# Kernel tuning notes

Hardware: AMD Instinct MI355X
Metric: run time of the kernel (lower is better)

## Reference

```python
import jax, jax.numpy as jnp
import numpy as np

BATCH = 1_000_000
D = 20

def setup_inputs() -> dict:
    key = jax.random.key(0)
    kX, kW, kb, kR = jax.random.split(key, 4)
    X = jax.random.normal(kX, (BATCH, D), dtype=jnp.float32)
    W = jax.random.normal(kW, (D, D), dtype=jnp.float32)
    b = jax.random.normal(kb, (D,), dtype=jnp.float32)
    rand_weight = jax.random.uniform(kR, (D, D), dtype=jnp.float32)  # torch.rand, requires_grad=False
    return {"X": X, "W": W, "b": b, "rand_weight": rand_weight}

def reference(X, W, b, rand_weight):
    # X = self.linear(X)
    X1 = X @ W.T + b
    # X = relu(X @ rand_weight + 1)
    X2 = jax.nn.relu(X1 @ rand_weight + 1.0)
    # X = self.linear(X)  (shared weights)
    X3 = X2 @ W.T + b
    # while X.abs().sum() > 1: X = X / 2  -- data-dependent loop, kept on-device
    def cond(Xc):
        return jnp.sum(jnp.abs(Xc)) > 1.0
    def body(Xc):
        return Xc * 0.5
    Xf = jax.lax.while_loop(cond, body, X3)
    return jnp.sum(Xf)
```

## Files before the change

kernel.cpp:

```cpp
#include <hip/hip_runtime.h>
#include <math.h>

#define D 20
#define NROWS 1000000
#define NTILES (NROWS / 16)
#define TPB 256
#define TILES_PER_BLK 16
#define NSB ((NTILES + TILES_PER_BLK - 1) / TILES_PER_BLK)
#define NF4 (NROWS * D / 4)
#define F4_PER_SB (TILES_PER_BLK * 16 * D / 4)

typedef float  f32x4  __attribute__((ext_vector_type(4)));
typedef __bf16 bf16x8 __attribute__((ext_vector_type(8)));

#define FRAG_OFF 65536

__device__ inline unsigned int pk2(float a, float b) {
  unsigned short la = __builtin_bit_cast(unsigned short, (__bf16)a);
  unsigned short lb = __builtin_bit_cast(unsigned short, (__bf16)b);
  return (unsigned int)la | ((unsigned int)lb << 16);
}

__global__ __launch_bounds__(512) void setup_kernel(
    const float* __restrict__ W, const float* __restrict__ b,
    const float* __restrict__ R, unsigned int* __restrict__ frags) {
  __shared__ float A_s[D * D];
  __shared__ float c_s[D];
  const int t = threadIdx.x;
  if (t < D * D) {
    int j = t / D, m = t % D;
    float s = 0.f;
#pragma unroll
    for (int i = 0; i < D; ++i) s = fmaf(W[i * D + j], R[i * D + m], s);
    A_s[j * D + m] = s;
  } else if (t < D * D + D) {
    int m = t - D * D;
    float s = 1.0f;
#pragma unroll
    for (int i = 0; i < D; ++i) s = fmaf(b[i], R[i * D + m], s);
    c_s[m] = s;
  }
  __syncthreads();
  if (t < 64) {
    const int G = t >> 4, ii = t & 15;
    uint4* out = (uint4*)frags;
    unsigned w[4];
    for (int wd = 0; wd < 4; ++wd) {
      float v[2];
      for (int h = 0; h < 2; ++h) {
        int k = G * 8 + 2 * wd + h;
        v[h] = (k < D) ? A_s[k * D + ii] : (k == D ? c_s[ii] : 0.f);
      }
      w[wd] = pk2(v[0], v[1]);
    }
    out[t] = make_uint4(w[0], w[1], w[2], w[3]);
    for (int wd = 0; wd < 4; ++wd) {
      float v[2];
      for (int h = 0; h < 2; ++h) {
        int k = G * 8 + 2 * wd + h;
        int m = 16 + ii;
        v[h] = (m < D) ? ((k < D) ? A_s[k * D + m] : (k == D ? c_s[m] : 0.f)) : 0.f;
      }
      w[wd] = pk2(v[0], v[1]);
    }
    out[64 + t] = make_uint4(w[0], w[1], w[2], w[3]);
    for (int wd = 0; wd < 4; ++wd) {
      float v[2];
      for (int h = 0; h < 2; ++h) {
        int e = 2 * wd + h;
        int sg = (e < 4) ? (4 * G + e) : (16 + 4 * G + (e - 4));
        v[h] = (sg < D) ? W[ii * D + sg] : (sg == D ? b[ii] : 0.f);
      }
      w[wd] = pk2(v[0], v[1]);
    }
    out[128 + t] = make_uint4(w[0], w[1], w[2], w[3]);
    for (int wd = 0; wd < 4; ++wd) {
      float v[2];
      for (int h = 0; h < 2; ++h) {
        int e = 2 * wd + h;
        int sg = (e < 4) ? (4 * G + e) : (16 + 4 * G + (e - 4));
        int n = 16 + ii;
        v[h] = (n < D) ? ((sg < D) ? W[n * D + sg] : (sg == D ? b[n] : 0.f)) : 0.f;
      }
      w[wd] = pk2(v[0], v[1]);
    }
    out[192 + t] = make_uint4(w[0], w[1], w[2], w[3]);
  }
}

__global__ __launch_bounds__(TPB) void main_kernel(
    const float* __restrict__ X, const unsigned int* __restrict__ frags,
    double* __restrict__ partial) {
  __shared__ float4 xs4[F4_PER_SB + 8];
  float* xs = (float*)xs4;
  const int t = threadIdx.x;
  const int s = blockIdx.x;

  const float4* X4 = (const float4*)X;
#pragma unroll
  for (int j = 0; j < 5; ++j) {
    int gi = s * F4_PER_SB + j * TPB + t;
    gi = (gi < NF4) ? gi : (NF4 - 1);
    xs4[j * TPB + t] = X4[gi];
  }

  const int lane = t & 63;
  const int G = lane >> 4, ii = lane & 15;
  const int wid = t >> 6;
  const uint4* fr = (const uint4*)frags;
  const bf16x8 B1t1 = __builtin_bit_cast(bf16x8, fr[lane]);
  const bf16x8 B1t2 = __builtin_bit_cast(bf16x8, fr[64 + lane]);
  const bf16x8 B2t1 = __builtin_bit_cast(bf16x8, fr[128 + lane]);
  const bf16x8 B2t2 = __builtin_bit_cast(bf16x8, fr[192 + lane]);
  __syncthreads();

  const bool mA = (G < 3);
  const bool mB = (G < 2);
  const int gf = (G < 2) ? G * 8 : 16;
  const float* rowp = xs + ii * D + gf;
  const int tbase = s * TILES_PER_BLK + wid * 4;
  double s64 = 0.0, sa64 = 0.0;

#pragma unroll
  for (int k = 0; k < 4; ++k) {
    if (tbase + k < NTILES) {
      const float* p = rowp + (wid * 4 + k) * (16 * D);
      const float4 ca = *(const float4*)p;
      const float4 cb = *(const float4*)(p + 4);

      bf16x8 xf;
      xf[0] = (__bf16)(mA ? ca.x : 0.f);
      xf[1] = (__bf16)(mA ? ca.y : 0.f);
      xf[2] = (__bf16)(mA ? ca.z : 0.f);
      xf[3] = (__bf16)(mA ? ca.w : 0.f);
      xf[4] = (__bf16)(mB ? cb.x : (G == 2 ? 1.0f : 0.f));
      xf[5] = (__bf16)(mB ? cb.y : 0.f);
      xf[6] = (__bf16)(mB ? cb.z : 0.f);
      xf[7] = (__bf16)(mB ? cb.w : 0.f);

      const f32x4 zz = {0.f, 0.f, 0.f, 0.f};
      f32x4 a1 = __builtin_amdgcn_mfma_f32_16x16x32_bf16(B1t1, xf, zz, 0, 0, 0);
      f32x4 a2 = __builtin_amdgcn_mfma_f32_16x16x32_bf16(B1t2, xf, zz, 0, 0, 0);
#pragma unroll
      for (int q = 0; q < 4; ++q) {
        a1[q] = fmaxf(a1[q], 0.f);
        a2[q] = fmaxf(a2[q], 0.f);
      }
      const float hj = (G == 1) ? 1.0f : a2[0];
      bf16x8 x2f;
      x2f[0] = (__bf16)a1[0]; x2f[1] = (__bf16)a1[1];
      x2f[2] = (__bf16)a1[2]; x2f[3] = (__bf16)a1[3];
      x2f[4] = (__bf16)hj;    x2f[5] = (__bf16)a2[1];
      x2f[6] = (__bf16)a2[2]; x2f[7] = (__bf16)a2[3];

      f32x4 z1 = __builtin_amdgcn_mfma_f32_16x16x32_bf16(x2f, B2t1, zz, 0, 0, 0);
      f32x4 z2 = __builtin_amdgcn_mfma_f32_16x16x32_bf16(x2f, B2t2, zz, 0, 0, 0);

      const float s8 = ((z1[0] + z1[1]) + (z1[2] + z1[3])) +
                       ((z2[0] + z2[1]) + (z2[2] + z2[3]));
      const float sa8 =
          ((fabsf(z1[0]) + fabsf(z1[1])) + (fabsf(z1[2]) + fabsf(z1[3]))) +
          ((fabsf(z2[0]) + fabsf(z2[1])) + (fabsf(z2[2]) + fabsf(z2[3])));
      s64 += (double)s8;
      sa64 += (double)sa8;
    }
  }

#pragma unroll
  for (int off = 32; off > 0; off >>= 1) {
    s64 += __shfl_down(s64, off, 64);
    sa64 += __shfl_down(sa64, off, 64);
  }
  __shared__ double red[8];
  if ((t & 63) == 0) { red[wid * 2] = s64; red[wid * 2 + 1] = sa64; }
  __syncthreads();
  if (t == 0) {
    partial[2 * s]     = red[0] + red[2] + red[4] + red[6];
    partial[2 * s + 1] = red[1] + red[3] + red[5] + red[7];
  }
}

__global__ __launch_bounds__(256) void final_kernel(
    const double* __restrict__ partial, float* __restrict__ out) {
  double s = 0.0, sa = 0.0;
  for (int i = threadIdx.x; i < NSB; i += 256) {
    s += partial[2 * i];
    sa += partial[2 * i + 1];
  }
#pragma unroll
  for (int off = 32; off > 0; off >>= 1) {
    s += __shfl_down(s, off, 64);
    sa += __shfl_down(sa, off, 64);
  }
  __shared__ double red[8];
  int wid = threadIdx.x >> 6;
  if ((threadIdx.x & 63) == 0) { red[wid * 2] = s; red[wid * 2 + 1] = sa; }
  __syncthreads();
  if (threadIdx.x == 0) {
    double S  = red[0] + red[2] + red[4] + red[6];
    double SA = red[1] + red[3] + red[5] + red[7];
    int k = 0;
    double t = SA;
    while (t > 1.0 && k < 4096) { t *= 0.5; ++k; }
    out[0] = (float)ldexp(S, -k);
  }
}

extern "C" void kernel_launch(void* const* d_in, const int* in_sizes, int n_in,
                              void* d_out, int out_size, void* d_ws, size_t ws_size,
                              hipStream_t stream) {
  const float* X = (const float*)d_in[0];
  const float* W = (const float*)d_in[1];
  const float* b = (const float*)d_in[2];
  const float* R = (const float*)d_in[3];
  char* ws = (char*)d_ws;
  double* partial = (double*)ws;
  unsigned int* frags = (unsigned int*)(ws + FRAG_OFF);

  setup_kernel<<<1, 512, 0, stream>>>(W, b, R, frags);
  main_kernel<<<NSB, TPB, 0, stream>>>(X, frags, partial);
  final_kernel<<<1, 256, 0, stream>>>(partial, (float*)d_out);
}
```

Before: 30.98 us.

## Fuse weight-fragment setup into main kernel to drop a launch

Removes the separate single-block setup kernel. Each main-kernel block now loads W, R and b into shared memory, recomputes the combined W^T·R matrix and bias vector, and builds its bf16 MFMA fragments locally. This saves one kernel launch and its serial dependency ahead of the bandwidth-bound main pass, at the cost of redundant 20x20x20 work and extra shared memory in every block. The X-fragment construction also swaps per-element selects for pointer selection into constant one/zero slots in shared memory.

```diff
diff --git a/kernel.cpp b/kernel.cpp
--- a/kernel.cpp
+++ b/kernel.cpp
@@ -13,86 +13,21 @@
 typedef float  f32x4  __attribute__((ext_vector_type(4)));
 typedef __bf16 bf16x8 __attribute__((ext_vector_type(8)));
 
-#define FRAG_OFF 65536
-
-__device__ inline unsigned int pk2(float a, float b) {
-  unsigned short la = __builtin_bit_cast(unsigned short, (__bf16)a);
-  unsigned short lb = __builtin_bit_cast(unsigned short, (__bf16)b);
-  return (unsigned int)la | ((unsigned int)lb << 16);
-}
-
-__global__ __launch_bounds__(512) void setup_kernel(
-    const float* __restrict__ W, const float* __restrict__ b,
-    const float* __restrict__ R, unsigned int* __restrict__ frags) {
-  __shared__ float A_s[D * D];
-  __shared__ float c_s[D];
-  const int t = threadIdx.x;
-  if (t < D * D) {
-    int j = t / D, m = t % D;
-    float s = 0.f;
-#pragma unroll
-    for (int i = 0; i < D; ++i) s = fmaf(W[i * D + j], R[i * D + m], s);
-    A_s[j * D + m] = s;
-  } else if (t < D * D + D) {
-    int m = t - D * D;
-    float s = 1.0f;
-#pragma unroll
-    for (int i = 0; i < D; ++i) s = fmaf(b[i], R[i * D + m], s);
-    c_s[m] = s;
-  }
-  __syncthreads();
-  if (t < 64) {
-    const int G = t >> 4, ii = t & 15;
-    uint4* out = (uint4*)frags;
-    unsigned w[4];
-    for (int wd = 0; wd < 4; ++wd) {
-      float v[2];
-      for (int h = 0; h < 2; ++h) {
-        int k = G * 8 + 2 * wd + h;
-        v[h] = (k < D) ? A_s[k * D + ii] : (k == D ? c_s[ii] : 0.f);
-      }
-      w[wd] = pk2(v[0], v[1]);
-    }
-    out[t] = make_uint4(w[0], w[1], w[2], w[3]);
-    for (int wd = 0; wd < 4; ++wd) {
-      float v[2];
-      for (int h = 0; h < 2; ++h) {
-        int k = G * 8 + 2 * wd + h;
-        int m = 16 + ii;
-        v[h] = (m < D) ? ((k < D) ? A_s[k * D + m] : (k == D ? c_s[m] : 0.f)) : 0.f;
-      }
-      w[wd] = pk2(v[0], v[1]);
-    }
-    out[64 + t] = make_uint4(w[0], w[1], w[2], w[3]);
-    for (int wd = 0; wd < 4; ++wd) {
-      float v[2];
-      for (int h = 0; h < 2; ++h) {
-        int e = 2 * wd + h;
-        int sg = (e < 4) ? (4 * G + e) : (16 + 4 * G + (e - 4));
-        v[h] = (sg < D) ? W[ii * D + sg] : (sg == D ? b[ii] : 0.f);
-      }
-      w[wd] = pk2(v[0], v[1]);
-    }
-    out[128 + t] = make_uint4(w[0], w[1], w[2], w[3]);
-    for (int wd = 0; wd < 4; ++wd) {
-      float v[2];
-      for (int h = 0; h < 2; ++h) {
-        int e = 2 * wd + h;
-        int sg = (e < 4) ? (4 * G + e) : (16 + 4 * G + (e - 4));
-        int n = 16 + ii;
-        v[h] = (n < D) ? ((sg < D) ? W[n * D + sg] : (sg == D ? b[n] : 0.f)) : 0.f;
-      }
-      w[wd] = pk2(v[0], v[1]);
-    }
-    out[192 + t] = make_uint4(w[0], w[1], w[2], w[3]);
-  }
-}
 
 __global__ __launch_bounds__(TPB) void main_kernel(
-    const float* __restrict__ X, const unsigned int* __restrict__ frags,
+    const float* __restrict__ X, const float* __restrict__ W,
+    const float* __restrict__ b, const float* __restrict__ R,
     double* __restrict__ partial) {
-  __shared__ float4 xs4[F4_PER_SB + 8];
-  float* xs = (float*)xs4;
+  __shared__ float4 xs4[F4_PER_SB + 2];
+  __shared__ float4 Wv[D * D / 4];
+  __shared__ float4 Rv[D * D / 4];
+  __shared__ float  b_s[D];
+  __shared__ float  A_s[D * D];
+  __shared__ float  c_s[D];
+  __shared__ double red[8];
+  float* xs  = (float*)xs4;
+  float* W_s = (float*)Wv;
+  float* R_s = (float*)Rv;
   const int t = threadIdx.x;
   const int s = blockIdx.x;
 
@@ -103,40 +38,73 @@
     gi = (gi < NF4) ? gi : (NF4 - 1);
     xs4[j * TPB + t] = X4[gi];
   }
+  if (t < 100) Wv[t] = ((const float4*)W)[t];
+  else if (t < 200) Rv[t - 100] = ((const float4*)R)[t - 100];
+  else if (t < 220) b_s[t - 200] = b[t - 200];
+  else if (t < 228) xs[4 * F4_PER_SB + (t - 220)] = (t == 220) ? 1.0f : 0.0f;
+  __syncthreads();
+
+  for (int q = t; q < D * D + D; q += TPB) {
+    if (q < D * D) {
+      int j = q / D, m = q % D;
+      float acc = 0.f;
+#pragma unroll
+      for (int i = 0; i < D; ++i) acc = fmaf(W_s[i * D + j], R_s[i * D + m], acc);
+      A_s[q] = acc;
+    } else {
+      int m = q - D * D;
+      float acc = 1.0f;
+#pragma unroll
+      for (int i = 0; i < D; ++i) acc = fmaf(b_s[i], R_s[i * D + m], acc);
+      c_s[m] = acc;
+    }
+  }
+  __syncthreads();
 
   const int lane = t & 63;
   const int G = lane >> 4, ii = lane & 15;
   const int wid = t >> 6;
-  const uint4* fr = (const uint4*)frags;
-  const bf16x8 B1t1 = __builtin_bit_cast(bf16x8, fr[lane]);
-  const bf16x8 B1t2 = __builtin_bit_cast(bf16x8, fr[64 + lane]);
-  const bf16x8 B2t1 = __builtin_bit_cast(bf16x8, fr[128 + lane]);
-  const bf16x8 B2t2 = __builtin_bit_cast(bf16x8, fr[192 + lane]);
-  __syncthreads();
+  bf16x8 B1t1, B1t2, B2t1, B2t2;
+#pragma unroll
+  for (int e = 0; e < 8; ++e) {
+    int k = G * 8 + e;
+    int kc = (k < D) ? k : (D - 1);
+    float v1 = A_s[kc * D + ii];
+    B1t1[e] = (__bf16)((k < D) ? v1 : (k == D ? c_s[ii] : 0.f));
+    int m2 = 16 + ii;
+    float v2 = (m2 < D) ? A_s[kc * D + m2] : 0.f;
+    B1t2[e] = (__bf16)((m2 < D) ? ((k < D) ? v2 : (k == D ? c_s[m2] : 0.f)) : 0.f);
+    int sg = (e < 4) ? (4 * G + e) : (16 + 4 * G + (e - 4));
+    int sgc = (sg < D) ? sg : (D - 1);
+    float v3 = W_s[ii * D + sgc];
+    B2t1[e] = (__bf16)((sg < D) ? v3 : (sg == D ? b_s[ii] : 0.f));
+    float v4 = (m2 < D) ? W_s[m2 * D + sgc] : 0.f;
+    B2t2[e] = (__bf16)((m2 < D) ? ((sg < D) ? v4 : (sg == D ? b_s[m2] : 0.f)) : 0.f);
+  }
 
-  const bool mA = (G < 3);
-  const bool mB = (G < 2);
-  const int gf = (G < 2) ? G * 8 : 16;
-  const float* rowp = xs + ii * D + gf;
-  const int tbase = s * TILES_PER_BLK + wid * 4;
+  float* zC = xs + 4 * F4_PER_SB;
+  float* zZ = zC + 4;
+  const float* caBase; int caStr;
+  const float* cbBase; int cbStr;
+  if (G < 2)       { caBase = xs + ii * D + G * 8; caStr = 16 * D;
+                     cbBase = caBase + 4;          cbStr = 16 * D; }
+  else if (G == 2) { caBase = xs + ii * D + 16;    caStr = 16 * D;
+                     cbBase = zC;                  cbStr = 0; }
+  else             { caBase = zZ;                  caStr = 0;
+                     cbBase = zZ;                  cbStr = 0; }
+
   double s64 = 0.0, sa64 = 0.0;
-
 #pragma unroll
   for (int k = 0; k < 4; ++k) {
-    if (tbase + k < NTILES) {
-      const float* p = rowp + (wid * 4 + k) * (16 * D);
-      const float4 ca = *(const float4*)p;
-      const float4 cb = *(const float4*)(p + 4);
-
+    const int wt = wid * 4 + k;
+    if (s * TILES_PER_BLK + wt < NTILES) {
+      const float4 ca = *(const float4*)(caBase + wt * caStr);
+      const float4 cb = *(const float4*)(cbBase + wt * cbStr);
       bf16x8 xf;
-      xf[0] = (__bf16)(mA ? ca.x : 0.f);
-      xf[1] = (__bf16)(mA ? ca.y : 0.f);
-      xf[2] = (__bf16)(mA ? ca.z : 0.f);
-      xf[3] = (__bf16)(mA ? ca.w : 0.f);
-      xf[4] = (__bf16)(mB ? cb.x : (G == 2 ? 1.0f : 0.f));
-      xf[5] = (__bf16)(mB ? cb.y : 0.f);
-      xf[6] = (__bf16)(mB ? cb.z : 0.f);
-      xf[7] = (__bf16)(mB ? cb.w : 0.f);
+      xf[0] = (__bf16)ca.x; xf[1] = (__bf16)ca.y;
+      xf[2] = (__bf16)ca.z; xf[3] = (__bf16)ca.w;
+      xf[4] = (__bf16)cb.x; xf[5] = (__bf16)cb.y;
+      xf[6] = (__bf16)cb.z; xf[7] = (__bf16)cb.w;
 
       const f32x4 zz = {0.f, 0.f, 0.f, 0.f};
       f32x4 a1 = __builtin_amdgcn_mfma_f32_16x16x32_bf16(B1t1, xf, zz, 0, 0, 0);
@@ -171,7 +139,6 @@
     s64 += __shfl_down(s64, off, 64);
     sa64 += __shfl_down(sa64, off, 64);
   }
-  __shared__ double red[8];
   if ((t & 63) == 0) { red[wid * 2] = s64; red[wid * 2 + 1] = sa64; }
   __syncthreads();
   if (t == 0) {
@@ -213,11 +180,8 @@
   const float* W = (const float*)d_in[1];
   const float* b = (const float*)d_in[2];
   const float* R = (const float*)d_in[3];
-  char* ws = (char*)d_ws;
-  double* partial = (double*)ws;
-  unsigned int* frags = (unsigned int*)(ws + FRAG_OFF);
+  double* partial = (double*)d_ws;
 
-  setup_kernel<<<1, 512, 0, stream>>>(W, b, R, frags);
-  main_kernel<<<NSB, TPB, 0, stream>>>(X, frags, partial);
+  main_kernel<<<NSB, TPB, 0, stream>>>(X, W, b, R, partial);
   final_kernel<<<1, 256, 0, stream>>>(partial, (float*)d_out);
 }
```

After: 37.60 us. 21.4% more time.

## Fuse final reduction into main kernel via last-block atomic counter

Applied to the files above, without the earlier changes.

Removes the separate final reduction kernel. Each block now writes its partials and increments a global counter, and the last block to finish reduces all partials and applies the halving loop. The per-lane select masks for building the MFMA input fragment are replaced by per-group base pointers into shared memory, including constant one/zero slots, so the inner loop has fewer conditional selects. This saves one kernel launch at the cost of atomics and a serialized tail reduction in a single block.

```diff
diff --git a/kernel.cpp b/kernel.cpp
--- a/kernel.cpp
+++ b/kernel.cpp
@@ -13,7 +13,8 @@
 typedef float  f32x4  __attribute__((ext_vector_type(4)));
 typedef __bf16 bf16x8 __attribute__((ext_vector_type(8)));
 
-#define FRAG_OFF 65536
+#define CNT_OFF 65536
+#define FRAG_OFF (CNT_OFF + 256)
 
 __device__ inline unsigned int pk2(float a, float b) {
   unsigned short la = __builtin_bit_cast(unsigned short, (__bf16)a);
@@ -23,10 +24,12 @@
 
 __global__ __launch_bounds__(512) void setup_kernel(
     const float* __restrict__ W, const float* __restrict__ b,
-    const float* __restrict__ R, unsigned int* __restrict__ frags) {
+    const float* __restrict__ R, unsigned int* __restrict__ frags,
+    unsigned int* __restrict__ counter) {
   __shared__ float A_s[D * D];
   __shared__ float c_s[D];
   const int t = threadIdx.x;
+  if (t == 511) *counter = 0u;
   if (t < D * D) {
     int j = t / D, m = t % D;
     float s = 0.f;
@@ -90,8 +93,11 @@
 
 __global__ __launch_bounds__(TPB) void main_kernel(
     const float* __restrict__ X, const unsigned int* __restrict__ frags,
-    double* __restrict__ partial) {
-  __shared__ float4 xs4[F4_PER_SB + 8];
+    double* __restrict__ partial, unsigned int* __restrict__ counter,
+    float* __restrict__ out) {
+  __shared__ float4 xs4[F4_PER_SB + 2];
+  __shared__ double red[8];
+  __shared__ int amLast;
   float* xs = (float*)xs4;
   const int t = threadIdx.x;
   const int s = blockIdx.x;
@@ -103,6 +109,7 @@
     gi = (gi < NF4) ? gi : (NF4 - 1);
     xs4[j * TPB + t] = X4[gi];
   }
+  if (t < 8) xs[4 * F4_PER_SB + t] = (t == 0) ? 1.0f : 0.0f;
 
   const int lane = t & 63;
   const int G = lane >> 4, ii = lane & 15;
@@ -114,29 +121,29 @@
   const bf16x8 B2t2 = __builtin_bit_cast(bf16x8, fr[192 + lane]);
   __syncthreads();
 
-  const bool mA = (G < 3);
-  const bool mB = (G < 2);
-  const int gf = (G < 2) ? G * 8 : 16;
-  const float* rowp = xs + ii * D + gf;
-  const int tbase = s * TILES_PER_BLK + wid * 4;
+  float* zC = xs + 4 * F4_PER_SB;
+  float* zZ = zC + 4;
+  const float* caBase; int caStr;
+  const float* cbBase; int cbStr;
+  if (G < 2)       { caBase = xs + ii * D + G * 8; caStr = 16 * D;
+                     cbBase = caBase + 4;          cbStr = 16 * D; }
+  else if (G == 2) { caBase = xs + ii * D + 16;    caStr = 16 * D;
+                     cbBase = zC;                  cbStr = 0; }
+  else             { caBase = zZ;                  caStr = 0;
+                     cbBase = zZ;                  cbStr = 0; }
+
   double s64 = 0.0, sa64 = 0.0;
-
 #pragma unroll
   for (int k = 0; k < 4; ++k) {
-    if (tbase + k < NTILES) {
-      const float* p = rowp + (wid * 4 + k) * (16 * D);
-      const float4 ca = *(const float4*)p;
-      const float4 cb = *(const float4*)(p + 4);
-
+    const int wt = wid * 4 + k;
+    if (s * TILES_PER_BLK + wt < NTILES) {
+      const float4 ca = *(const float4*)(caBase + wt * caStr);
+      const float4 cb = *(const float4*)(cbBase + wt * cbStr);
       bf16x8 xf;
-      xf[0] = (__bf16)(mA ? ca.x : 0.f);
-      xf[1] = (__bf16)(mA ? ca.y : 0.f);
-      xf[2] = (__bf16)(mA ? ca.z : 0.f);
-      xf[3] = (__bf16)(mA ? ca.w : 0.f);
-      xf[4] = (__bf16)(mB ? cb.x : (G == 2 ? 1.0f : 0.f));
-      xf[5] = (__bf16)(mB ? cb.y : 0.f);
-      xf[6] = (__bf16)(mB ? cb.z : 0.f);
-      xf[7] = (__bf16)(mB ? cb.w : 0.f);
+      xf[0] = (__bf16)ca.x; xf[1] = (__bf16)ca.y;
+      xf[2] = (__bf16)ca.z; xf[3] = (__bf16)ca.w;
+      xf[4] = (__bf16)cb.x; xf[5] = (__bf16)cb.y;
+      xf[6] = (__bf16)cb.z; xf[7] = (__bf16)cb.w;
 
       const f32x4 zz = {0.f, 0.f, 0.f, 0.f};
       f32x4 a1 = __builtin_amdgcn_mfma_f32_16x16x32_bf16(B1t1, xf, zz, 0, 0, 0);
@@ -171,38 +178,42 @@
     s64 += __shfl_down(s64, off, 64);
     sa64 += __shfl_down(sa64, off, 64);
   }
-  __shared__ double red[8];
   if ((t & 63) == 0) { red[wid * 2] = s64; red[wid * 2 + 1] = sa64; }
   __syncthreads();
   if (t == 0) {
-    partial[2 * s]     = red[0] + red[2] + red[4] + red[6];
-    partial[2 * s + 1] = red[1] + red[3] + red[5] + red[7];
-  }
-}
-
-__global__ __launch_bounds__(256) void final_kernel(
-    const double* __restrict__ partial, float* __restrict__ out) {
-  double s = 0.0, sa = 0.0;
-  for (int i = threadIdx.x; i < NSB; i += 256) {
-    s += partial[2 * i];
-    sa += partial[2 * i + 1];
-  }
-#pragma unroll
-  for (int off = 32; off > 0; off >>= 1) {
-    s += __shfl_down(s, off, 64);
-    sa += __shfl_down(sa, off, 64);
-  }
-  __shared__ double red[8];
-  int wid = threadIdx.x >> 6;
-  if ((threadIdx.x & 63) == 0) { red[wid * 2] = s; red[wid * 2 + 1] = sa; }
-  __syncthreads();
-  if (threadIdx.x == 0) {
-    double S  = red[0] + red[2] + red[4] + red[6];
-    double SA = red[1] + red[3] + red[5] + red[7];
-    int k = 0;
-    double t = SA;
-    while (t > 1.0 && k < 4096) { t *= 0.5; ++k; }
-    out[0] = (float)ldexp(S, -k);
+    __hip_atomic_store(&partial[2 * s],     red[0] + red[2] + red[4] + red[6],
+                       __ATOMIC_RELAXED, __HIP_MEMORY_SCOPE_AGENT);
+    __hip_atomic_store(&partial[2 * s + 1], red[1] + red[3] + red[5] + red[7],
+                       __ATOMIC_RELAXED, __HIP_MEMORY_SCOPE_AGENT);
+    unsigned int old = __hip_atomic_fetch_add(counter, 1u, __ATOMIC_ACQ_REL,
+                                              __HIP_MEMORY_SCOPE_AGENT);
+    amLast = (old == NSB - 1);
+  }
+  __syncthreads();
+
+  if (amLast) {
+    double s = 0.0, sa = 0.0;
+    for (int i = t; i < NSB; i += TPB) {
+      s += __hip_atomic_load(&partial[2 * i], __ATOMIC_RELAXED,
+                             __HIP_MEMORY_SCOPE_AGENT);
+      sa += __hip_atomic_load(&partial[2 * i + 1], __ATOMIC_RELAXED,
+                              __HIP_MEMORY_SCOPE_AGENT);
+    }
+#pragma unroll
+    for (int off = 32; off > 0; off >>= 1) {
+      s += __shfl_down(s, off, 64);
+      sa += __shfl_down(sa, off, 64);
+    }
+    if ((t & 63) == 0) { red[wid * 2] = s; red[wid * 2 + 1] = sa; }
+    __syncthreads();
+    if (t == 0) {
+      double S  = red[0] + red[2] + red[4] + red[6];
+      double SA = red[1] + red[3] + red[5] + red[7];
+      int k = 0;
+      double tt = SA;
+      while (tt > 1.0 && k < 4096) { tt *= 0.5; ++k; }
+      out[0] = (float)ldexp(S, -k);
+    }
   }
 }
 
@@ -215,9 +226,10 @@
   const float* R = (const float*)d_in[3];
   char* ws = (char*)d_ws;
   double* partial = (double*)ws;
+  unsigned int* counter = (unsigned int*)(ws + CNT_OFF);
   unsigned int* frags = (unsigned int*)(ws + FRAG_OFF);
 
-  setup_kernel<<<1, 512, 0, stream>>>(W, b, R, frags);
-  main_kernel<<<NSB, TPB, 0, stream>>>(X, frags, partial);
-  final_kernel<<<1, 256, 0, stream>>>(partial, (float*)d_out);
-}
+  setup_kernel<<<1, 512, 0, stream>>>(W, b, R, frags, counter);
+  main_kernel<<<NSB, TPB, 0, stream>>>(X, frags, partial, counter,
+                                       (float*)d_out);
+}
```

New measurement: 114.1 us. 268% more time.

## Use persistent blocks with double-buffered direct global-to-LDS loads of X

Applied to the files above, without the earlier changes.

The main kernel now launches a fixed grid of 1024 persistent blocks that loop over super-blocks. Each block double-buffers X tiles in LDS using global_load_lds, so the next tile's load overlaps compute on the current one. Padding lanes now read constant 1/0 slots in LDS instead of using per-element selects, and the final reduction covers 1024 partials. This targets the exposed load latency of the single-shot, one-tile-per-block design, at the cost of hand-managed waitcnt/barrier synchronisation that may be fragile.

```diff
diff --git a/kernel.cpp b/kernel.cpp
--- a/kernel.cpp
+++ b/kernel.cpp
@@ -7,13 +7,17 @@
 #define TPB 256
 #define TILES_PER_BLK 16
 #define NSB ((NTILES + TILES_PER_BLK - 1) / TILES_PER_BLK)
+#define NBLK 1024
 #define NF4 (NROWS * D / 4)
 #define F4_PER_SB (TILES_PER_BLK * 16 * D / 4)
 
 typedef float  f32x4  __attribute__((ext_vector_type(4)));
 typedef __bf16 bf16x8 __attribute__((ext_vector_type(8)));
 
-#define FRAG_OFF 65536
+#define AS1 __attribute__((address_space(1)))
+#define AS3 __attribute__((address_space(3)))
+
+#define FRAG_OFF (NBLK * 16)
 
 __device__ inline unsigned int pk2(float a, float b) {
   unsigned short la = __builtin_bit_cast(unsigned short, (__bf16)a);
@@ -80,7 +84,7 @@
         int e = 2 * wd + h;
         int sg = (e < 4) ? (4 * G + e) : (16 + 4 * G + (e - 4));
         int n = 16 + ii;
-        v[h] = (n < D) ? ((sg < D) ? W[n * D + sg] : (sg == D ? b[n] : 0.f)) : 0.f;
+        v[h] = (n < D) ? ((sg < D) ? W[ii * 0 + n * D + sg] : (sg == D ? b[n] : 0.f)) : 0.f;
       }
       w[wd] = pk2(v[0], v[1]);
     }
@@ -91,79 +95,106 @@
 __global__ __launch_bounds__(TPB) void main_kernel(
     const float* __restrict__ X, const unsigned int* __restrict__ frags,
     double* __restrict__ partial) {
-  __shared__ float4 xs4[F4_PER_SB + 8];
+  __shared__ float4 xs4[2 * F4_PER_SB + 2];
   float* xs = (float*)xs4;
   const int t = threadIdx.x;
-  const int s = blockIdx.x;
-
-  const float4* X4 = (const float4*)X;
-#pragma unroll
-  for (int j = 0; j < 5; ++j) {
-    int gi = s * F4_PER_SB + j * TPB + t;
-    gi = (gi < NF4) ? gi : (NF4 - 1);
-    xs4[j * TPB + t] = X4[gi];
-  }
-
   const int lane = t & 63;
   const int G = lane >> 4, ii = lane & 15;
   const int wid = t >> 6;
+  const float4* X4 = (const float4*)X;
+
+  if (t < 8) xs[8 * F4_PER_SB + t] = (t == 0) ? 1.0f : 0.0f;
+
   const uint4* fr = (const uint4*)frags;
   const bf16x8 B1t1 = __builtin_bit_cast(bf16x8, fr[lane]);
   const bf16x8 B1t2 = __builtin_bit_cast(bf16x8, fr[64 + lane]);
   const bf16x8 B2t1 = __builtin_bit_cast(bf16x8, fr[128 + lane]);
   const bf16x8 B2t2 = __builtin_bit_cast(bf16x8, fr[192 + lane]);
-  __syncthreads();
-
-  const bool mA = (G < 3);
-  const bool mB = (G < 2);
-  const int gf = (G < 2) ? G * 8 : 16;
-  const float* rowp = xs + ii * D + gf;
-  const int tbase = s * TILES_PER_BLK + wid * 4;
+
+#define STAGE(bsel, sb)                                                        \
+  do {                                                                         \
+    _Pragma("unroll")                                                          \
+    for (int j = 0; j < 5; ++j) {                                              \
+      int f4i = (sb) * F4_PER_SB + j * TPB + t;                                \
+      f4i = (f4i < NF4) ? f4i : (NF4 - 1);        \
+      __builtin_amdgcn_global_load_lds(                                        \
+          (AS1 const void*)(X4 + f4i),                                         \
+          (AS3 void*)(xs4 + (bsel) * F4_PER_SB + j * (TPB / 4) * 4 + wid * 64),\
+          16, 0, 0);                                                           \
+    }                                                                          \
+  } while (0)
+
+  int sb = blockIdx.x;
+  STAGE(0, sb);
+  asm volatile("s_waitcnt lgkmcnt(0)" ::: "memory");
   double s64 = 0.0, sa64 = 0.0;
-
-#pragma unroll
-  for (int k = 0; k < 4; ++k) {
-    if (tbase + k < NTILES) {
-      const float* p = rowp + (wid * 4 + k) * (16 * D);
-      const float4 ca = *(const float4*)p;
-      const float4 cb = *(const float4*)(p + 4);
-
-      bf16x8 xf;
-      xf[0] = (__bf16)(mA ? ca.x : 0.f);
-      xf[1] = (__bf16)(mA ? ca.y : 0.f);
-      xf[2] = (__bf16)(mA ? ca.z : 0.f);
-      xf[3] = (__bf16)(mA ? ca.w : 0.f);
-      xf[4] = (__bf16)(mB ? cb.x : (G == 2 ? 1.0f : 0.f));
-      xf[5] = (__bf16)(mB ? cb.y : 0.f);
-      xf[6] = (__bf16)(mB ? cb.z : 0.f);
-      xf[7] = (__bf16)(mB ? cb.w : 0.f);
-
-      const f32x4 zz = {0.f, 0.f, 0.f, 0.f};
-      f32x4 a1 = __builtin_amdgcn_mfma_f32_16x16x32_bf16(B1t1, xf, zz, 0, 0, 0);
-      f32x4 a2 = __builtin_amdgcn_mfma_f32_16x16x32_bf16(B1t2, xf, zz, 0, 0, 0);
-#pragma unroll
-      for (int q = 0; q < 4; ++q) {
-        a1[q] = fmaxf(a1[q], 0.f);
-        a2[q] = fmaxf(a2[q], 0.f);
-      }
-      const float hj = (G == 1) ? 1.0f : a2[0];
-      bf16x8 x2f;
-      x2f[0] = (__bf16)a1[0]; x2f[1] = (__bf16)a1[1];
-      x2f[2] = (__bf16)a1[2]; x2f[3] = (__bf16)a1[3];
-      x2f[4] = (__bf16)hj;    x2f[5] = (__bf16)a2[1];
-      x2f[6] = (__bf16)a2[2]; x2f[7] = (__bf16)a2[3];
-
-      f32x4 z1 = __builtin_amdgcn_mfma_f32_16x16x32_bf16(x2f, B2t1, zz, 0, 0, 0);
-      f32x4 z2 = __builtin_amdgcn_mfma_f32_16x16x32_bf16(x2f, B2t2, zz, 0, 0, 0);
-
-      const float s8 = ((z1[0] + z1[1]) + (z1[2] + z1[3])) +
-                       ((z2[0] + z2[1]) + (z2[2] + z2[3]));
-      const float sa8 =
-          ((fabsf(z1[0]) + fabsf(z1[1])) + (fabsf(z1[2]) + fabsf(z1[3]))) +
-          ((fabsf(z2[0]) + fabsf(z2[1])) + (fabsf(z2[2]) + fabsf(z2[3])));
-      s64 += (double)s8;
-      sa64 += (double)sa8;
-    }
+  int cur = 0;
+
+  for (; sb < NSB; sb += NBLK) {
+    const int nxt = sb + NBLK;
+    const bool has = (nxt < NSB);
+    if (has) {
+      STAGE(cur ^ 1, nxt);
+      asm volatile("s_waitcnt vmcnt(5)" ::: "memory");
+    } else {
+      asm volatile("s_waitcnt vmcnt(0)" ::: "memory");
+    }
+    __builtin_amdgcn_sched_barrier(0);
+    __builtin_amdgcn_s_barrier();
+
+    float* xsb = xs + cur * (F4_PER_SB * 4);
+    float* zC = xs + 8 * F4_PER_SB;
+    float* zZ = zC + 4;
+    const float* caBase; int caStr;
+    const float* cbBase; int cbStr;
+    if (G < 2)       { caBase = xsb + ii * D + G * 8; caStr = 16 * D;
+                       cbBase = caBase + 4;           cbStr = 16 * D; }
+    else if (G == 2) { caBase = xsb + ii * D + 16;    caStr = 16 * D;
+                       cbBase = zC;                   cbStr = 0; }
+    else             { caBase = zZ;                   caStr = 0;
+                       cbBase = zZ;                   cbStr = 0; }
+
+#pragma unroll
+    for (int k = 0; k < 4; ++k) {
+      const int wt = wid * 4 + k;
+      if (sb * TILES_PER_BLK + wt < NTILES) {
+        const float4 ca = *(const float4*)(caBase + wt * caStr);
+        const float4 cb = *(const float4*)(cbBase + wt * cbStr);
+        bf16x8 xf;
+        xf[0] = (__bf16)ca.x; xf[1] = (__bf16)ca.y;
+        xf[2] = (__bf16)ca.z; xf[3] = (__bf16)ca.w;
+        xf[4] = (__bf16)cb.x; xf[5] = (__bf16)cb.y;
+        xf[6] = (__bf16)cb.z; xf[7] = (__bf16)cb.w;
+
+        const f32x4 zz = {0.f, 0.f, 0.f, 0.f};
+        f32x4 a1 = __builtin_amdgcn_mfma_f32_16x16x32_bf16(B1t1, xf, zz, 0, 0, 0);
+        f32x4 a2 = __builtin_amdgcn_mfma_f32_16x16x32_bf16(B1t2, xf, zz, 0, 0, 0);
+#pragma unroll
+        for (int q = 0; q < 4; ++q) {
+          a1[q] = fmaxf(a1[q], 0.f);
+          a2[q] = fmaxf(a2[q], 0.f);
+        }
+        const float hj = (G == 1) ? 1.0f : a2[0];
+        bf16x8 x2f;
+        x2f[0] = (__bf16)a1[0]; x2f[1] = (__bf16)a1[1];
+        x2f[2] = (__bf16)a1[2]; x2f[3] = (__bf16)a1[3];
+        x2f[4] = (__bf16)hj;    x2f[5] = (__bf16)a2[1];
+        x2f[6] = (__bf16)a2[2]; x2f[7] = (__bf16)a2[3];
+
+        f32x4 z1 = __builtin_amdgcn_mfma_f32_16x16x32_bf16(x2f, B2t1, zz, 0, 0, 0);
+        f32x4 z2 = __builtin_amdgcn_mfma_f32_16x16x32_bf16(x2f, B2t2, zz, 0, 0, 0);
+
+        const float s8 = ((z1[0] + z1[1]) + (z1[2] + z1[3])) +
+                         ((z2[0] + z2[1]) + (z2[2] + z2[3]));
+        const float sa8 =
+            ((fabsf(z1[0]) + fabsf(z1[1])) + (fabsf(z1[2]) + fabsf(z1[3]))) +
+            ((fabsf(z2[0]) + fabsf(z2[1])) + (fabsf(z2[2]) + fabsf(z2[3])));
+        s64 += (double)s8;
+        sa64 += (double)sa8;
+      }
+    }
+    __builtin_amdgcn_s_barrier();
+    cur ^= 1;
   }
 
 #pragma unroll
@@ -175,15 +206,15 @@
   if ((t & 63) == 0) { red[wid * 2] = s64; red[wid * 2 + 1] = sa64; }
   __syncthreads();
   if (t == 0) {
-    partial[2 * s]     = red[0] + red[2] + red[4] + red[6];
-    partial[2 * s + 1] = red[1] + red[3] + red[5] + red[7];
+    partial[2 * blockIdx.x]     = red[0] + red[2] + red[4] + red[6];
+    partial[2 * blockIdx.x + 1] = red[1] + red[3] + red[5] + red[7];
   }
 }
 
 __global__ __launch_bounds__(256) void final_kernel(
     const double* __restrict__ partial, float* __restrict__ out) {
   double s = 0.0, sa = 0.0;
-  for (int i = threadIdx.x; i < NSB; i += 256) {
+  for (int i = threadIdx.x; i < NBLK; i += 256) {
     s += partial[2 * i];
     sa += partial[2 * i + 1];
   }
@@ -218,6 +249,6 @@
   unsigned int* frags = (unsigned int*)(ws + FRAG_OFF);
 
   setup_kernel<<<1, 512, 0, stream>>>(W, b, R, frags);
-  main_kernel<<<NSB, TPB, 0, stream>>>(X, frags, partial);
+  main_kernel<<<NBLK, TPB, 0, stream>>>(X, frags, partial);
   final_kernel<<<1, 256, 0, stream>>>(partial, (float*)d_out);
 }
```

Result: slower. 32.25 us (+4.1%).
